# Kernel optimization log

Measured on AMD Instinct MI355X. Metric: run time of the kernel, lower is better.

## Reference

```python
import jax, jax.numpy as jnp
import numpy as np

N = 50000      # nodes
E = 800000     # edges
D = 128        # in_dim == out_dim
H = 8          # heads
DH = D // H    # head dim = 16
BN_EPS = 1e-5


def batch_norm(x, gamma, beta):
    # BatchNorm1d in training mode: biased variance over the node/batch axis.
    mu = jnp.mean(x, axis=0)
    var = jnp.mean((x - mu) ** 2, axis=0)
    return (x - mu) * jax.lax.rsqrt(var + BN_EPS) * gamma + beta


def setup_inputs() -> dict:
    key = jax.random.key(0)
    ks = jax.random.split(key, 16)
    inp = {
        'src': jax.random.randint(ks[0], (E,), 0, N),
        'dst': jax.random.randint(ks[1], (E,), 0, N),
        'h': jax.random.normal(ks[2], (N, D), jnp.float32),
        'e': jax.random.normal(ks[3], (E, D), jnp.float32),
        'h_in': jax.random.normal(ks[4], (N, D), jnp.float32),  # unused: overwritten by h in forward
        # attention projections (bias=False)
        'Wq': jax.random.normal(ks[5], (D, D), jnp.float32) / np.sqrt(D),
        'Wk': jax.random.normal(ks[6], (D, D), jnp.float32) / np.sqrt(D),
        'Wv': jax.random.normal(ks[7], (D, D), jnp.float32) / np.sqrt(D),
        'We': jax.random.normal(ks[8], (D, D), jnp.float32) / np.sqrt(D),
        # sdp_layer (bias=True)
        'W_sdp': jax.random.normal(ks[9], (D, D), jnp.float32) / np.sqrt(D),
        'b_sdp': jnp.zeros((D,), jnp.float32),
        # FFN out_h / out_h_2
        'W_h1': jax.random.normal(ks[10], (D, 2 * D), jnp.float32) / np.sqrt(D),
        'b_h1': jnp.zeros((2 * D,), jnp.float32),
        'W_h2': jax.random.normal(ks[11], (2 * D, D), jnp.float32) / np.sqrt(2 * D),
        'b_h2': jnp.zeros((D,), jnp.float32),
        # batch_norm_1 (shared across both BN applications)
        'bn_gamma': jnp.ones((D,), jnp.float32),
        'bn_beta': jnp.zeros((D,), jnp.float32),
    }
    return inp


def reference(src, dst, h, e, h_in, Wq, Wk, Wv, We, W_sdp, b_sdp,
              W_h1, b_h1, W_h2, b_h2, bn_gamma, bn_beta):
    h_res = h  # h_in = h inside forward

    # --- MultiHeadAttention (default path: all edges real, sum aggregation) ---
    q = (h @ Wq).reshape(N, H, DH)
    k = (h @ Wk).reshape(N, H, DH)
    v = (h @ Wv).reshape(N, H, DH)   # v = v_linear(h_in) with h_in == h
    ef = (e @ We).reshape(E, H, DH)

    # src_dot_dst -> scaling -> imp_exp_attn: elementwise K_src*Q_dst / sqrt(dh) * E
    score = (k[src] * q[dst]) / np.sqrt(DH) * ef          # [E, H, DH]
    # exp('score'): exp(clamp(sum_d score, -5, 5)), keepdim
    score_soft = jnp.exp(jnp.clip(score.sum(-1), -5.0, 5.0))[..., None]  # [E, H, 1]

    aV = jax.ops.segment_sum(v[src] * score_soft, dst, num_segments=N)   # [N, H, DH]
    z = jax.ops.segment_sum(score_soft, dst, num_segments=N)             # [N, H, 1]
    h_attn = (aV / (z + 1e-6)).reshape(N, D)

    # --- EncoderLayer post-attention (dropout=0 -> identity) ---
    hx = h_attn @ W_sdp + b_sdp
    hx = h_res + hx
    hx = batch_norm(hx, bn_gamma, bn_beta)

    h_in2 = hx
    ff = jax.nn.relu(hx @ W_h1 + b_h1) @ W_h2 + b_h2
    hx = h_in2 + ff
    hx = batch_norm(hx, bn_gamma, bn_beta)

    # edge_learning=False: e returned unchanged
    return hx, e
```

## Files before the change

### kernel.cpp

```cpp
#include <hip/hip_runtime.h>
#include <hip/hip_bf16.h>
#include <math.h>

#define N_NODES 50000
#define E_EDGES 800000
#define D_DIM   128
#define H_HEADS 8

typedef __attribute__((ext_vector_type(8))) short short8;
typedef __attribute__((ext_vector_type(4))) float f32x4;
typedef unsigned int   uint_t;
typedef unsigned short ushort_t;

static __device__ __forceinline__ float4 ldg4(const float* p) {
    return *reinterpret_cast<const float4*>(p);
}
static __device__ __forceinline__ ushort_t f2bf(float x) {
    union { float f; uint_t u; } v; v.f = x;
    uint_t r = v.u + 0x7fffu + ((v.u >> 16) & 1u);
    return (ushort_t)(r >> 16);
}
static __device__ __forceinline__ float bf2f(ushort_t b) {
    union { uint_t u; float f; } v; v.u = ((uint_t)b) << 16;
    return v.f;
}
static __device__ __forceinline__ uint_t pk(float lo, float hi) {
    return (uint_t)f2bf(lo) | ((uint_t)f2bf(hi) << 16);
}

__global__ void hist_kernel(const int* __restrict__ dst, int* __restrict__ hist) {
    int i = blockIdx.x * blockDim.x + threadIdx.x;
    if (i < E_EDGES) atomicAdd(&hist[dst[i]], 1);
}

__global__ __launch_bounds__(1024) void scan_kernel(const int* __restrict__ cnt,
                                                    int* __restrict__ start,
                                                    int* __restrict__ cursor) {
    __shared__ int sh[1024];
    const int t = threadIdx.x;
    const int CPT = (N_NODES + 1023) / 1024;
    int lo = t * CPT;
    int hi = lo + CPT; if (hi > N_NODES) hi = N_NODES; if (lo > N_NODES) lo = N_NODES;
    int s = 0;
    for (int i = lo; i < hi; i++) s += cnt[i];
    sh[t] = s;
    __syncthreads();
    for (int off = 1; off < 1024; off <<= 1) {
        int v = (t >= off) ? sh[t - off] : 0;
        __syncthreads();
        sh[t] += v;
        __syncthreads();
    }
    int run = sh[t] - s;
    for (int i = lo; i < hi; i++) {
        start[i]  = run;
        cursor[i] = run;
        run += cnt[i];
    }
    if (t == 1023) start[N_NODES] = sh[1023];
}

__global__ void scatter_kernel(const int* __restrict__ src, const int* __restrict__ dst,
                               int* __restrict__ cursor,
                               int* __restrict__ rank, int* __restrict__ srcs) {
    int i = blockIdx.x * blockDim.x + threadIdx.x;
    if (i < E_EDGES) {
        int p = atomicAdd(&cursor[dst[i]], 1);
        rank[i] = p;
        srcs[p] = src[i];
    }
}

__global__ __launch_bounds__(256) void prep_weights(const float* __restrict__ Wq,
                                                    const float* __restrict__ Wk,
                                                    const float* __restrict__ Wv,
                                                    const float* __restrict__ We,
                                                    const float* __restrict__ Wsdp,
                                                    const float* __restrict__ Wh1,
                                                    const float* __restrict__ Wh2,
                                                    ushort_t* __restrict__ prep) {
    const int b = blockIdx.x;
    const float* W; int ld, cb, kc;
    if (b < 6)       { W = (b < 2 ? Wq : (b < 4 ? Wk : Wv)); ld = 128; cb = 0; kc = b & 1; }
    else if (b < 8)  { W = We;   ld = 128; cb = 0;            kc = b - 6; }
    else if (b < 10) { W = Wsdp; ld = 128; cb = 0;            kc = b - 8; }
    else if (b < 14) { W = Wh1;  ld = 256; cb = (b - 10) >> 1; kc = (b - 10) & 1; }
    else             { W = Wh2;  ld = 128; cb = 0;            kc = b - 14; }
    char* tile = (char*)(prep + (size_t)b * 8192);
    for (int i = threadIdx.x; i < 8192; i += 256) {
        int col = i >> 6, kl = i & 63;
        int k = kc * 64 + kl;
        float v = W[(size_t)k * ld + cb * 128 + col];
        int byte = (col * 128 + kl * 2) ^ ((col & 7) << 4);
        *(ushort_t*)(tile + byte) = f2bf(v);
    }
}

__global__ __launch_bounds__(256) void prep_we_frag(const float* __restrict__ We,
                                                    ushort_t* __restrict__ WeF) {
    int slot = blockIdx.x * 256 + threadIdx.x;
    if (slot < 2048) {
        int lane = slot & 63;
        int kc   = (slot >> 6) & 3;
        int cg   = slot >> 8;
        int col  = cg * 16 + (lane & 15);
        int kb   = kc * 32 + ((lane >> 4) << 3);
#pragma unroll
        for (int j = 0; j < 8; j++)
            WeF[slot * 8 + j] = f2bf(We[(size_t)(kb + j) * 128 + col]);
    }
}

template<int ROWS, int OBF>
__global__ __launch_bounds__(256) void gemm_bf16(const float* __restrict__ A,
                                                 int M, int K,
                                                 const ushort_t* __restrict__ Bt, int nkc,
                                                 const float* __restrict__ bias,
                                                 const float* __restrict__ resid,
                                                 void* __restrict__ Cv, int ldc,
                                                 size_t cbStride, int doRelu) {
    constexpr int MI  = ROWS / 32;
    constexpr int TPR = 256 / ROWS;
    constexpr int KPT = 64 / TPR;
    __shared__ __align__(16) unsigned char As[ROWS * 128];
    __shared__ __align__(16) unsigned char Bs[16384];
    const int tid  = threadIdx.x;
    const int lane = tid & 63;
    const int wid  = tid >> 6;
    const int wr   = wid >> 1;
    const int wc   = wid & 1;
    const int cb   = blockIdx.y;
    const int row0 = blockIdx.x * ROWS;

    f32x4 acc[MI][4];
#pragma unroll
    for (int i = 0; i < MI; i++)
#pragma unroll
        for (int j = 0; j < 4; j++) acc[i][j] = (f32x4){0.f, 0.f, 0.f, 0.f};

    for (int kc = 0; kc < nkc; kc++) {
        __syncthreads();
        {
            int row = tid / TPR;
            int kl0 = (tid % TPR) * KPT;
            int gr  = row0 + row;
            float4 v4[KPT / 4];
            if (gr < M) {
                const float* ap = &A[(size_t)gr * K + kc * 64 + kl0];
#pragma unroll
                for (int j = 0; j < KPT / 4; j++) v4[j] = ldg4(ap + 4 * j);
            } else {
#pragma unroll
                for (int j = 0; j < KPT / 4; j++) v4[j] = make_float4(0.f, 0.f, 0.f, 0.f);
            }
            int s = (row & 7) << 4;
#pragma unroll
            for (int j = 0; j < KPT / 8; j++) {
                uint4 w;
                w.x = pk(v4[2 * j].x, v4[2 * j].y);
                w.y = pk(v4[2 * j].z, v4[2 * j].w);
                w.z = pk(v4[2 * j + 1].x, v4[2 * j + 1].y);
                w.w = pk(v4[2 * j + 1].z, v4[2 * j + 1].w);
                int byte = (row * 128 + (kl0 + 8 * j) * 2) ^ s;
                *(uint4*)(As + byte) = w;
            }
        }
        {
            const uint4* gB = (const uint4*)(Bt + (size_t)(cb * nkc + kc) * 8192);
#pragma unroll
            for (int j = 0; j < 4; j++) {
                int idx = j * 256 + tid;
                ((uint4*)Bs)[idx] = gB[idx];
            }
        }
        __syncthreads();
#pragma unroll
        for (int k0 = 0; k0 < 64; k0 += 32) {
            short8 a[MI], b[4];
#pragma unroll
            for (int mi = 0; mi < MI; mi++) {
                int row = wr * (ROWS / 2) + mi * 16 + (lane & 15);
                int byte = (row * 128 + k0 * 2 + (lane >> 4) * 16) ^ ((row & 7) << 4);
                a[mi] = *(const short8*)(As + byte);
            }
#pragma unroll
            for (int ni = 0; ni < 4; ni++) {
                int col = wc * 64 + ni * 16 + (lane & 15);
                int byte = (col * 128 + k0 * 2 + (lane >> 4) * 16) ^ ((col & 7) << 4);
                b[ni] = *(const short8*)(Bs + byte);
            }
#pragma unroll
            for (int mi = 0; mi < MI; mi++)
#pragma unroll
                for (int ni = 0; ni < 4; ni++)
                    acc[mi][ni] = __builtin_amdgcn_mfma_f32_16x16x32_bf16(a[mi], b[ni], acc[mi][ni], 0, 0, 0);
        }
    }
#pragma unroll
    for (int mi = 0; mi < MI; mi++) {
#pragma unroll
        for (int r = 0; r < 4; r++) {
            int row = row0 + wr * (ROWS / 2) + mi * 16 + ((lane >> 4) << 2) + r;
            if (row < M) {
#pragma unroll
                for (int ni = 0; ni < 4; ni++) {
                    int col = wc * 64 + ni * 16 + (lane & 15);
                    float v = acc[mi][ni][r];
                    if (bias) v += bias[cb * 128 + col];
                    if (doRelu) v = fmaxf(v, 0.f);
                    if (resid) v += resid[(size_t)row * ldc + col];
                    if (OBF) {
                        ((ushort_t*)Cv)[cb * cbStride + (size_t)row * ldc + col] = f2bf(v);
                    } else {
                        ((float*)Cv)[cb * cbStride + (size_t)row * ldc + col] = v;
                    }
                }
            }
        }
    }
}

__global__ __launch_bounds__(512, 8) void edge_mfma(const float* __restrict__ e,
                                                    const int* __restrict__ src,
                                                    const int* __restrict__ dst,
                                                    const ushort_t* __restrict__ Qm,
                                                    const ushort_t* __restrict__ Km,
                                                    const ushort_t* __restrict__ WeF,
                                                    const int* __restrict__ rank,
                                                    float* __restrict__ S,
                                                    float* __restrict__ out_e) {
    __shared__ __align__(16) unsigned char Asm[16384];
    __shared__ float sm[64][8];
    const int tid  = threadIdx.x;
    const int lane = tid & 63;
    const int wid  = tid >> 6;
    const int wr   = wid >> 2;
    const int wc   = wid & 3;
    const int e0   = blockIdx.x * 64;

    {
        int row = tid >> 3;
        int c0  = (tid & 7) * 16;
        const float* ep = &e[(size_t)(e0 + row) * 128 + c0];
        float*       op = &out_e[(size_t)(e0 + row) * 128 + c0];
        float4 v4[4];
#pragma unroll
        for (int j = 0; j < 4; j++) v4[j] = ldg4(ep + 4 * j);
#pragma unroll
        for (int j = 0; j < 4; j++) *(float4*)(op + 4 * j) = v4[j];
        int chunk = c0 >> 6;
        int klb   = (c0 & 63) * 2;
        int s     = (row & 7) << 4;
        uint4 w0, w1;
        w0.x = pk(v4[0].x, v4[0].y); w0.y = pk(v4[0].z, v4[0].w);
        w0.z = pk(v4[1].x, v4[1].y); w0.w = pk(v4[1].z, v4[1].w);
        w1.x = pk(v4[2].x, v4[2].y); w1.y = pk(v4[2].z, v4[2].w);
        w1.z = pk(v4[3].x, v4[3].y); w1.w = pk(v4[3].z, v4[3].w);
        *(uint4*)(Asm + chunk * 8192 + ((row * 128 + klb) ^ s))      = w0;
        *(uint4*)(Asm + chunk * 8192 + ((row * 128 + klb + 16) ^ s)) = w1;
    }
    __syncthreads();

    f32x4 acc[2][2];
#pragma unroll
    for (int i = 0; i < 2; i++)
#pragma unroll
        for (int j = 0; j < 2; j++) acc[i][j] = (f32x4){0.f, 0.f, 0.f, 0.f};

#pragma unroll
    for (int k0 = 0; k0 < 128; k0 += 32) {
        int chunk = k0 >> 6;
        int klb   = (k0 & 63) * 2;
        int kc    = k0 >> 5;
        short8 a[2];
#pragma unroll
        for (int mi = 0; mi < 2; mi++) {
            int arow = wr * 32 + mi * 16 + (lane & 15);
            int byte = chunk * 8192 + ((arow * 128 + klb + (lane >> 4) * 16) ^ ((arow & 7) << 4));
            a[mi] = *(const short8*)(Asm + byte);
        }
#pragma unroll
        for (int ni = 0; ni < 2; ni++) {
            int cg = wc * 2 + ni;
            short8 b = *(const short8*)(WeF + ((size_t)((cg * 4 + kc) * 64 + lane)) * 8);
#pragma unroll
            for (int mi = 0; mi < 2; mi++)
                acc[mi][ni] = __builtin_amdgcn_mfma_f32_16x16x32_bf16(a[mi], b, acc[mi][ni], 0, 0, 0);
        }
    }

#pragma unroll
    for (int mi = 0; mi < 2; mi++) {
        int rows[4], sidx[4], didx[4];
#pragma unroll
        for (int r = 0; r < 4; r++) {
            rows[r] = e0 + wr * 32 + mi * 16 + ((lane >> 4) << 2) + r;
            sidx[r] = src[rows[r]];
            didx[r] = dst[rows[r]];
        }
#pragma unroll
        for (int ni = 0; ni < 2; ni++) {
            int head = wc * 2 + ni;
            int col  = head * 16 + (lane & 15);
            float pv[4];
#pragma unroll
            for (int r = 0; r < 4; r++) {
                float kv = bf2f(Km[(size_t)sidx[r] * 128 + col]);
                float qv = bf2f(Qm[(size_t)didx[r] * 128 + col]);
                pv[r] = acc[mi][ni][r] * kv * qv;
            }
#pragma unroll
            for (int off = 1; off < 16; off <<= 1)
#pragma unroll
                for (int r = 0; r < 4; r++) pv[r] += __shfl_xor(pv[r], off, 64);
            if ((lane & 15) == 0) {
#pragma unroll
                for (int r = 0; r < 4; r++) {
                    float v = fminf(fmaxf(0.25f * pv[r], -5.f), 5.f);
                    sm[rows[r] - e0][head] = __expf(v);
                }
            }
        }
    }
    __syncthreads();
    if (tid < 64) {
        int rk = rank[e0 + tid];
        float4 a0 = *(const float4*)&sm[tid][0];
        float4 a1 = *(const float4*)&sm[tid][4];
        *(float4*)&S[(size_t)rk * 8]     = a0;
        *(float4*)&S[(size_t)rk * 8 + 4] = a1;
    }
}

__global__ __launch_bounds__(128) void agg_kernel(const ushort_t* __restrict__ V,
                                                  const float* __restrict__ S,
                                                  const int* __restrict__ start,
                                                  const int* __restrict__ srcs,
                                                  float* __restrict__ HA) {
    const int n = blockIdx.x;
    const int t = threadIdx.x;
    const int h = t >> 4;
    const int s0 = start[n];
    const int s1 = start[n + 1];
    float acc = 0.f, z = 0.f;
    int i = s0;
    for (; i + 4 <= s1; i += 4) {
        int  n0 = srcs[i], n1 = srcs[i + 1], n2 = srcs[i + 2], n3 = srcs[i + 3];
        float sv0 = S[(size_t)i * 8 + h];
        float sv1 = S[(size_t)(i + 1) * 8 + h];
        float sv2 = S[(size_t)(i + 2) * 8 + h];
        float sv3 = S[(size_t)(i + 3) * 8 + h];
        float v0 = bf2f(V[(size_t)n0 * 128 + t]);
        float v1 = bf2f(V[(size_t)n1 * 128 + t]);
        float v2 = bf2f(V[(size_t)n2 * 128 + t]);
        float v3 = bf2f(V[(size_t)n3 * 128 + t]);
        acc = fmaf(sv0, v0, acc); acc = fmaf(sv1, v1, acc);
        acc = fmaf(sv2, v2, acc); acc = fmaf(sv3, v3, acc);
        z += sv0 + sv1 + sv2 + sv3;
    }
    for (; i < s1; i++) {
        int ns = srcs[i];
        float sv = S[(size_t)i * 8 + h];
        acc = fmaf(sv, bf2f(V[(size_t)ns * 128 + t]), acc);
        z += sv;
    }
    HA[(size_t)n * 128 + t] = acc / (z + 1e-6f);
}

__global__ __launch_bounds__(256) void bn_stats(const float* __restrict__ X,
                                                float* __restrict__ sums) {
    __shared__ float s1[256], s2[256];
    const int tid = threadIdx.x;
    float a1 = 0.f, a2 = 0.f;
    const size_t total = (size_t)N_NODES * 128;
    for (size_t i = (size_t)blockIdx.x * 256 + tid; i < total; i += (size_t)gridDim.x * 256) {
        float v = X[i];
        a1 += v;
        a2 += v * v;
    }
    s1[tid] = a1; s2[tid] = a2;
    __syncthreads();
    if (tid < 128) {
        a1 = s1[tid] + s1[tid + 128];
        a2 = s2[tid] + s2[tid + 128];
        atomicAdd(&sums[tid], a1);
        atomicAdd(&sums[128 + tid], a2);
    }
}

__global__ void bn_finalize(const float* __restrict__ sums, float* __restrict__ mu_rstd) {
    int c = threadIdx.x;
    float mu  = sums[c] * (1.f / (float)N_NODES);
    float var = sums[128 + c] * (1.f / (float)N_NODES) - mu * mu;
    mu_rstd[c]       = mu;
    mu_rstd[128 + c] = rsqrtf(var + 1e-5f);
}

__global__ __launch_bounds__(256) void bn_apply(const float* __restrict__ X,
                                                const float* __restrict__ mu_rstd,
                                                const float* __restrict__ gamma,
                                                const float* __restrict__ beta,
                                                float* __restrict__ Y) {
    const size_t total = (size_t)N_NODES * 128;
    const size_t step = (size_t)gridDim.x * blockDim.x * 4;
    for (size_t i = ((size_t)blockIdx.x * blockDim.x + threadIdx.x) * 4; i < total; i += step) {
        float4 x = ldg4(&X[i]);
        int c = (int)(i & 127);
        float4 y;
        y.x = (x.x - mu_rstd[c + 0]) * mu_rstd[128 + c + 0] * gamma[c + 0] + beta[c + 0];
        y.y = (x.y - mu_rstd[c + 1]) * mu_rstd[128 + c + 1] * gamma[c + 1] + beta[c + 1];
        y.z = (x.z - mu_rstd[c + 2]) * mu_rstd[128 + c + 2] * gamma[c + 2] + beta[c + 2];
        y.w = (x.w - mu_rstd[c + 3]) * mu_rstd[128 + c + 3] * gamma[c + 3] + beta[c + 3];
        *reinterpret_cast<float4*>(&Y[i]) = y;
    }
}

extern "C" void kernel_launch(void* const* d_in, const int* in_sizes, int n_in,
                              void* d_out, int out_size, void* d_ws, size_t ws_size,
                              hipStream_t stream) {
    (void)in_sizes; (void)n_in; (void)out_size; (void)ws_size;
    const int*   src   = (const int*)d_in[0];
    const int*   dst   = (const int*)d_in[1];
    const float* h     = (const float*)d_in[2];
    const float* e     = (const float*)d_in[3];
    const float* Wq    = (const float*)d_in[5];
    const float* Wk    = (const float*)d_in[6];
    const float* Wv    = (const float*)d_in[7];
    const float* We    = (const float*)d_in[8];
    const float* Wsdp  = (const float*)d_in[9];
    const float* bsdp  = (const float*)d_in[10];
    const float* Wh1   = (const float*)d_in[11];
    const float* bh1   = (const float*)d_in[12];
    const float* Wh2   = (const float*)d_in[13];
    const float* bh2   = (const float*)d_in[14];
    const float* gamma = (const float*)d_in[15];
    const float* beta  = (const float*)d_in[16];
    float* out = (float*)d_out;

    float* ws = (float*)d_ws;
    const size_t NM = (size_t)N_NODES * 128;
    float* Qb    = ws;
    float* Kb    = ws + NM;
    float* Vb    = ws + 2 * NM;
    float* Sb    = ws + 3 * NM;
    float* T1    = ws + 4 * NM;
    float* STATS = ws + 6 * NM;
    int* hist   = (int*)(STATS + 1024);
    int* startp = hist + N_NODES;
    int* cursor = startp + N_NODES + 1;
    ushort_t* prep = (ushort_t*)(((uintptr_t)(cursor + N_NODES) + 255) & ~(uintptr_t)255);
    ushort_t* WeF  = prep + (size_t)18 * 8192;

    ushort_t* Q16 = (ushort_t*)Qb;
    ushort_t* K16 = Q16 + NM;
    ushort_t* V16 = Q16 + 2 * NM;

    int* rank = (int*)T1;
    int* srcs = rank + E_EDGES;

    float* sums1 = STATS;
    float* mr1   = STATS + 256;
    float* sums2 = STATS + 512;
    float* mr2   = STATS + 768;

    prep_weights<<<18, 256, 0, stream>>>(Wq, Wk, Wv, We, Wsdp, Wh1, Wh2, prep);
    prep_we_frag<<<8, 256, 0, stream>>>(We, WeF);

    hipMemsetAsync(STATS, 0, (1024 + N_NODES) * sizeof(float), stream);

    hist_kernel<<<(E_EDGES + 255) / 256, 256, 0, stream>>>(dst, hist);
    scan_kernel<<<1, 1024, 0, stream>>>(hist, startp, cursor);
    scatter_kernel<<<(E_EDGES + 255) / 256, 256, 0, stream>>>(src, dst, cursor, rank, srcs);

    const int rt128 = (N_NODES + 127) / 128;
    const int rt64  = (N_NODES + 63) / 64;

    gemm_bf16<128, 1><<<dim3(rt128, 3), 256, 0, stream>>>(h, N_NODES, 128, prep, 2,
                                                          nullptr, nullptr, Q16, 128, NM, 0);

    edge_mfma<<<E_EDGES / 64, 512, 0, stream>>>(e, src, dst, Q16, K16, WeF,
                                                rank, Sb, out + NM);

    agg_kernel<<<N_NODES, 128, 0, stream>>>(V16, Sb, startp, srcs, Vb);

    gemm_bf16<64, 0><<<dim3(rt64, 1), 256, 0, stream>>>(Vb, N_NODES, 128, prep + (size_t)8 * 8192, 2,
                                                        bsdp, h, Kb, 128, 0, 0);

    bn_stats<<<512, 256, 0, stream>>>(Kb, sums1);
    bn_finalize<<<1, 128, 0, stream>>>(sums1, mr1);
    bn_apply<<<2048, 256, 0, stream>>>(Kb, mr1, gamma, beta, Qb);

    gemm_bf16<128, 0><<<dim3(rt128, 2), 256, 0, stream>>>(Qb, N_NODES, 128, prep + (size_t)10 * 8192, 2,
                                                          bh1, nullptr, T1, 256, 128, 1);
    gemm_bf16<64, 0><<<dim3(rt64, 1), 256, 0, stream>>>(T1, N_NODES, 256, prep + (size_t)14 * 8192, 4,
                                                        bh2, Qb, Kb, 128, 0, 0);

    bn_stats<<<512, 256, 0, stream>>>(Kb, sums2);
    bn_finalize<<<1, 128, 0, stream>>>(sums2, mr2);
    bn_apply<<<2048, 256, 0, stream>>>(Kb, mr2, gamma, beta, out);
}
```

Baseline: 800.2 us.

## Make edge kernel persistent over four tiles with double-buffered LDS prefetch

Each edge block now walks four 64-edge tiles instead of one. It keeps two LDS staging buffers and issues the global load of the next tile's edge features and rank while the current tile's MFMA and gather work runs. The goal is to hide global-load latency and cut per-block launch and sync overhead. In exchange, LDS use doubles, there are four times fewer blocks, and the launch-bounds occupancy hint drops from 8 to 6.

After: 1.007 ms. +25.9%, slower.

```diff
diff --git a/kernel.cpp b/kernel.cpp
--- a/kernel.cpp
+++ b/kernel.cpp
@@ -6,6 +6,7 @@
 #define E_EDGES 800000
 #define D_DIM   128
 #define H_HEADS 8
+#define ETILES  4
 
 typedef __attribute__((ext_vector_type(8))) short short8;
 typedef __attribute__((ext_vector_type(4))) float f32x4;
@@ -220,7 +221,21 @@
     }
 }
 
-__global__ __launch_bounds__(512, 8) void edge_mfma(const float* __restrict__ e,
+static __device__ __forceinline__ void stage_tile(unsigned char* buf, int row, int c0,
+                                                  const float4* v4) {
+    int chunk = c0 >> 6;
+    int klb   = (c0 & 63) * 2;
+    int s     = (row & 7) << 4;
+    uint4 w0, w1;
+    w0.x = pk(v4[0].x, v4[0].y); w0.y = pk(v4[0].z, v4[0].w);
+    w0.z = pk(v4[1].x, v4[1].y); w0.w = pk(v4[1].z, v4[1].w);
+    w1.x = pk(v4[2].x, v4[2].y); w1.y = pk(v4[2].z, v4[2].w);
+    w1.z = pk(v4[3].x, v4[3].y); w1.w = pk(v4[3].z, v4[3].w);
+    *(uint4*)(buf + chunk * 8192 + ((row * 128 + klb) ^ s))      = w0;
+    *(uint4*)(buf + chunk * 8192 + ((row * 128 + klb + 16) ^ s)) = w1;
+}
+
+__global__ __launch_bounds__(512, 6) void edge_mfma(const float* __restrict__ e,
                                                     const int* __restrict__ src,
                                                     const int* __restrict__ dst,
                                                     const ushort_t* __restrict__ Qm,
@@ -229,106 +244,119 @@
                                                     const int* __restrict__ rank,
                                                     float* __restrict__ S,
                                                     float* __restrict__ out_e) {
-    __shared__ __align__(16) unsigned char Asm[16384];
+    __shared__ __align__(16) unsigned char Asm[2][16384];
     __shared__ float sm[64][8];
     const int tid  = threadIdx.x;
     const int lane = tid & 63;
     const int wid  = tid >> 6;
     const int wr   = wid >> 2;
     const int wc   = wid & 3;
-    const int e0   = blockIdx.x * 64;
-
+    const int row  = tid >> 3;
+    const int c0   = (tid & 7) * 16;
+    const int base = blockIdx.x * (64 * ETILES);
+
+    int rk = (tid < 64) ? rank[base + tid] : 0;
     {
-        int row = tid >> 3;
-        int c0  = (tid & 7) * 16;
-        const float* ep = &e[(size_t)(e0 + row) * 128 + c0];
-        float*       op = &out_e[(size_t)(e0 + row) * 128 + c0];
+        const float* ep = &e[(size_t)(base + row) * 128 + c0];
         float4 v4[4];
 #pragma unroll
         for (int j = 0; j < 4; j++) v4[j] = ldg4(ep + 4 * j);
+        float* op = &out_e[(size_t)(base + row) * 128 + c0];
 #pragma unroll
         for (int j = 0; j < 4; j++) *(float4*)(op + 4 * j) = v4[j];
-        int chunk = c0 >> 6;
-        int klb   = (c0 & 63) * 2;
-        int s     = (row & 7) << 4;
-        uint4 w0, w1;
-        w0.x = pk(v4[0].x, v4[0].y); w0.y = pk(v4[0].z, v4[0].w);
-        w0.z = pk(v4[1].x, v4[1].y); w0.w = pk(v4[1].z, v4[1].w);
-        w1.x = pk(v4[2].x, v4[2].y); w1.y = pk(v4[2].z, v4[2].w);
-        w1.z = pk(v4[3].x, v4[3].y); w1.w = pk(v4[3].z, v4[3].w);
-        *(uint4*)(Asm + chunk * 8192 + ((row * 128 + klb) ^ s))      = w0;
-        *(uint4*)(Asm + chunk * 8192 + ((row * 128 + klb + 16) ^ s)) = w1;
-    }
-    __syncthreads();
-
-    f32x4 acc[2][2];
-#pragma unroll
-    for (int i = 0; i < 2; i++)
-#pragma unroll
-        for (int j = 0; j < 2; j++) acc[i][j] = (f32x4){0.f, 0.f, 0.f, 0.f};
-
-#pragma unroll
-    for (int k0 = 0; k0 < 128; k0 += 32) {
-        int chunk = k0 >> 6;
-        int klb   = (k0 & 63) * 2;
-        int kc    = k0 >> 5;
-        short8 a[2];
+        stage_tile(Asm[0], row, c0, v4);
+    }
+
+#pragma unroll 1
+    for (int t = 0; t < ETILES; t++) {
+        const int e0 = base + t * 64;
+        __syncthreads();
+
+        float4 nv[4];
+        if (t + 1 < ETILES) {
+            const float* ep = &e[(size_t)(e0 + 64 + row) * 128 + c0];
+#pragma unroll
+            for (int j = 0; j < 4; j++) nv[j] = ldg4(ep + 4 * j);
+        }
+        int rk_cur = rk;
+        if (t + 1 < ETILES && tid < 64) rk = rank[e0 + 64 + tid];
+
+        f32x4 acc[2][2];
+#pragma unroll
+        for (int i = 0; i < 2; i++)
+#pragma unroll
+            for (int j = 0; j < 2; j++) acc[i][j] = (f32x4){0.f, 0.f, 0.f, 0.f};
+        const unsigned char* buf = Asm[t & 1];
+#pragma unroll
+        for (int k0 = 0; k0 < 128; k0 += 32) {
+            int chunk = k0 >> 6;
+            int klb   = (k0 & 63) * 2;
+            int kc    = k0 >> 5;
+            short8 a[2];
+#pragma unroll
+            for (int mi = 0; mi < 2; mi++) {
+                int arow = wr * 32 + mi * 16 + (lane & 15);
+                int byte = chunk * 8192 + ((arow * 128 + klb + (lane >> 4) * 16) ^ ((arow & 7) << 4));
+                a[mi] = *(const short8*)(buf + byte);
+            }
+#pragma unroll
+            for (int ni = 0; ni < 2; ni++) {
+                int cg = wc * 2 + ni;
+                short8 b = *(const short8*)(WeF + ((size_t)((cg * 4 + kc) * 64 + lane)) * 8);
+#pragma unroll
+                for (int mi = 0; mi < 2; mi++)
+                    acc[mi][ni] = __builtin_amdgcn_mfma_f32_16x16x32_bf16(a[mi], b, acc[mi][ni], 0, 0, 0);
+            }
+        }
+
 #pragma unroll
         for (int mi = 0; mi < 2; mi++) {
-            int arow = wr * 32 + mi * 16 + (lane & 15);
-            int byte = chunk * 8192 + ((arow * 128 + klb + (lane >> 4) * 16) ^ ((arow & 7) << 4));
-            a[mi] = *(const short8*)(Asm + byte);
-        }
-#pragma unroll
-        for (int ni = 0; ni < 2; ni++) {
-            int cg = wc * 2 + ni;
-            short8 b = *(const short8*)(WeF + ((size_t)((cg * 4 + kc) * 64 + lane)) * 8);
-#pragma unroll
-            for (int mi = 0; mi < 2; mi++)
-                acc[mi][ni] = __builtin_amdgcn_mfma_f32_16x16x32_bf16(a[mi], b, acc[mi][ni], 0, 0, 0);
-        }
-    }
-
-#pragma unroll
-    for (int mi = 0; mi < 2; mi++) {
-        int rows[4], sidx[4], didx[4];
-#pragma unroll
-        for (int r = 0; r < 4; r++) {
-            rows[r] = e0 + wr * 32 + mi * 16 + ((lane >> 4) << 2) + r;
-            sidx[r] = src[rows[r]];
-            didx[r] = dst[rows[r]];
-        }
-#pragma unroll
-        for (int ni = 0; ni < 2; ni++) {
-            int head = wc * 2 + ni;
-            int col  = head * 16 + (lane & 15);
-            float pv[4];
+            int rows[4], sidx[4], didx[4];
 #pragma unroll
             for (int r = 0; r < 4; r++) {
-                float kv = bf2f(Km[(size_t)sidx[r] * 128 + col]);
-                float qv = bf2f(Qm[(size_t)didx[r] * 128 + col]);
-                pv[r] = acc[mi][ni][r] * kv * qv;
-            }
-#pragma unroll
-            for (int off = 1; off < 16; off <<= 1)
-#pragma unroll
-                for (int r = 0; r < 4; r++) pv[r] += __shfl_xor(pv[r], off, 64);
-            if ((lane & 15) == 0) {
+                rows[r] = e0 + wr * 32 + mi * 16 + ((lane >> 4) << 2) + r;
+                sidx[r] = src[rows[r]];
+                didx[r] = dst[rows[r]];
+            }
+#pragma unroll
+            for (int ni = 0; ni < 2; ni++) {
+                int head = wc * 2 + ni;
+                int col  = head * 16 + (lane & 15);
+                float pv[4];
 #pragma unroll
                 for (int r = 0; r < 4; r++) {
-                    float v = fminf(fmaxf(0.25f * pv[r], -5.f), 5.f);
-                    sm[rows[r] - e0][head] = __expf(v);
+                    float kv = bf2f(Km[(size_t)sidx[r] * 128 + col]);
+                    float qv = bf2f(Qm[(size_t)didx[r] * 128 + col]);
+                    pv[r] = acc[mi][ni][r] * kv * qv;
                 }
-            }
-        }
-    }
-    __syncthreads();
-    if (tid < 64) {
-        int rk = rank[e0 + tid];
-        float4 a0 = *(const float4*)&sm[tid][0];
-        float4 a1 = *(const float4*)&sm[tid][4];
-        *(float4*)&S[(size_t)rk * 8]     = a0;
-        *(float4*)&S[(size_t)rk * 8 + 4] = a1;
+#pragma unroll
+                for (int off = 1; off < 16; off <<= 1)
+#pragma unroll
+                    for (int r = 0; r < 4; r++) pv[r] += __shfl_xor(pv[r], off, 64);
+                if ((lane & 15) == 0) {
+#pragma unroll
+                    for (int r = 0; r < 4; r++) {
+                        float v = fminf(fmaxf(0.25f * pv[r], -5.f), 5.f);
+                        sm[rows[r] - e0][head] = __expf(v);
+                    }
+                }
+            }
+        }
+        __syncthreads();
+
+        if (tid < 64) {
+            float4 a0 = *(const float4*)&sm[tid][0];
+            float4 a1 = *(const float4*)&sm[tid][4];
+            *(float4*)&S[(size_t)rk_cur * 8]     = a0;
+            *(float4*)&S[(size_t)rk_cur * 8 + 4] = a1;
+        }
+
+        if (t + 1 < ETILES) {
+            float* op = &out_e[(size_t)(e0 + 64 + row) * 128 + c0];
+#pragma unroll
+            for (int j = 0; j < 4; j++) *(float4*)(op + 4 * j) = nv[j];
+            stage_tile(Asm[(t + 1) & 1], row, c0, nv);
+        }
     }
 }
 
@@ -478,8 +506,8 @@
     gemm_bf16<128, 1><<<dim3(rt128, 3), 256, 0, stream>>>(h, N_NODES, 128, prep, 2,
                                                           nullptr, nullptr, Q16, 128, NM, 0);
 
-    edge_mfma<<<E_EDGES / 64, 512, 0, stream>>>(e, src, dst, Q16, K16, WeF,
-                                                rank, Sb, out + NM);
+    edge_mfma<<<E_EDGES / (64 * ETILES), 512, 0, stream>>>(e, src, dst, Q16, K16, WeF,
+                                                           rank, Sb, out + NM);
 
     agg_kernel<<<N_NODES, 128, 0, stream>>>(V16, Sb, startp, srcs, Vb);
 
```

## Fuse BN statistics into GEMM epilogues and store intermediates in bf16

Applied to the files above, without the earlier changes.

The BatchNorm column sums and sums of squares are now accumulated in the epilogues of the sdp and FFN2 GEMMs, so the two standalone bn_stats passes are gone. The aggregation output, the normalized activations and the FFN hidden layer are stored as bf16, and the GEMM loads bf16 A and residual inputs directly, which roughly halves intermediate memory traffic. The aggregation kernel now maps one wave per node with packed bf16 pairs, and bn_finalize folds gamma and beta into a single scale and shift. In exchange, the bf16 intermediates and residual lose precision, and per-block shared and global float atomics change the order of summation.

New measurement: 754.6 us. -5.7%, faster.

```diff
diff --git a/kernel.cpp b/kernel.cpp
--- a/kernel.cpp
+++ b/kernel.cpp
@@ -111,19 +111,21 @@
     }
 }
 
-template<int ROWS, int OBF>
-__global__ __launch_bounds__(256) void gemm_bf16(const float* __restrict__ A,
+template<int ROWS, int OBF, int ABF, int RBF, int SADD>
+__global__ __launch_bounds__(256) void gemm_bf16(const void* __restrict__ Av,
                                                  int M, int K,
                                                  const ushort_t* __restrict__ Bt, int nkc,
                                                  const float* __restrict__ bias,
-                                                 const float* __restrict__ resid,
+                                                 const void* __restrict__ residv,
                                                  void* __restrict__ Cv, int ldc,
-                                                 size_t cbStride, int doRelu) {
+                                                 size_t cbStride, int doRelu,
+                                                 float* __restrict__ sums) {
     constexpr int MI  = ROWS / 32;
     constexpr int TPR = 256 / ROWS;
     constexpr int KPT = 64 / TPR;
     __shared__ __align__(16) unsigned char As[ROWS * 128];
     __shared__ __align__(16) unsigned char Bs[16384];
+    __shared__ float csum[128], csq[128];
     const int tid  = threadIdx.x;
     const int lane = tid & 63;
     const int wid  = tid >> 6;
@@ -132,6 +134,8 @@
     const int cb   = blockIdx.y;
     const int row0 = blockIdx.x * ROWS;
 
+    if (SADD && tid < 128) { csum[tid] = 0.f; csq[tid] = 0.f; }
+
     f32x4 acc[MI][4];
 #pragma unroll
     for (int i = 0; i < MI; i++)
@@ -144,25 +148,37 @@
             int row = tid / TPR;
             int kl0 = (tid % TPR) * KPT;
             int gr  = row0 + row;
-            float4 v4[KPT / 4];
-            if (gr < M) {
-                const float* ap = &A[(size_t)gr * K + kc * 64 + kl0];
-#pragma unroll
-                for (int j = 0; j < KPT / 4; j++) v4[j] = ldg4(ap + 4 * j);
+            int s = (row & 7) << 4;
+            if (ABF) {
+                const ushort_t* A16 = (const ushort_t*)Av;
+#pragma unroll
+                for (int j = 0; j < KPT / 8; j++) {
+                    uint4 w = make_uint4(0, 0, 0, 0);
+                    if (gr < M) w = *(const uint4*)(&A16[(size_t)gr * K + kc * 64 + kl0 + 8 * j]);
+                    int byte = (row * 128 + (kl0 + 8 * j) * 2) ^ s;
+                    *(uint4*)(As + byte) = w;
+                }
             } else {
-#pragma unroll
-                for (int j = 0; j < KPT / 4; j++) v4[j] = make_float4(0.f, 0.f, 0.f, 0.f);
-            }
-            int s = (row & 7) << 4;
-#pragma unroll
-            for (int j = 0; j < KPT / 8; j++) {
-                uint4 w;
-                w.x = pk(v4[2 * j].x, v4[2 * j].y);
-                w.y = pk(v4[2 * j].z, v4[2 * j].w);
-                w.z = pk(v4[2 * j + 1].x, v4[2 * j + 1].y);
-                w.w = pk(v4[2 * j + 1].z, v4[2 * j + 1].w);
-                int byte = (row * 128 + (kl0 + 8 * j) * 2) ^ s;
-                *(uint4*)(As + byte) = w;
+                const float* A = (const float*)Av;
+                float4 v4[KPT / 4];
+                if (gr < M) {
+                    const float* ap = &A[(size_t)gr * K + kc * 64 + kl0];
+#pragma unroll
+                    for (int j = 0; j < KPT / 4; j++) v4[j] = ldg4(ap + 4 * j);
+                } else {
+#pragma unroll
+                    for (int j = 0; j < KPT / 4; j++) v4[j] = make_float4(0.f, 0.f, 0.f, 0.f);
+                }
+#pragma unroll
+                for (int j = 0; j < KPT / 8; j++) {
+                    uint4 w;
+                    w.x = pk(v4[2 * j].x, v4[2 * j].y);
+                    w.y = pk(v4[2 * j].z, v4[2 * j].w);
+                    w.z = pk(v4[2 * j + 1].x, v4[2 * j + 1].y);
+                    w.w = pk(v4[2 * j + 1].z, v4[2 * j + 1].w);
+                    int byte = (row * 128 + (kl0 + 8 * j) * 2) ^ s;
+                    *(uint4*)(As + byte) = w;
+                }
             }
         }
         {
@@ -196,6 +212,9 @@
                     acc[mi][ni] = __builtin_amdgcn_mfma_f32_16x16x32_bf16(a[mi], b[ni], acc[mi][ni], 0, 0, 0);
         }
     }
+
+    float colS[4] = {0.f, 0.f, 0.f, 0.f};
+    float colQ[4] = {0.f, 0.f, 0.f, 0.f};
 #pragma unroll
     for (int mi = 0; mi < MI; mi++) {
 #pragma unroll
@@ -208,14 +227,28 @@
                     float v = acc[mi][ni][r];
                     if (bias) v += bias[cb * 128 + col];
                     if (doRelu) v = fmaxf(v, 0.f);
-                    if (resid) v += resid[(size_t)row * ldc + col];
-                    if (OBF) {
-                        ((ushort_t*)Cv)[cb * cbStride + (size_t)row * ldc + col] = f2bf(v);
-                    } else {
-                        ((float*)Cv)[cb * cbStride + (size_t)row * ldc + col] = v;
+                    if (residv) {
+                        if (RBF) v += bf2f(((const ushort_t*)residv)[(size_t)row * ldc + col]);
+                        else     v += ((const float*)residv)[(size_t)row * ldc + col];
                     }
+                    if (SADD) { colS[ni] += v; colQ[ni] += v * v; }
+                    if (OBF) ((ushort_t*)Cv)[cb * cbStride + (size_t)row * ldc + col] = f2bf(v);
+                    else     ((float*)Cv)[cb * cbStride + (size_t)row * ldc + col] = v;
                 }
             }
+        }
+    }
+    if (SADD) {
+#pragma unroll
+        for (int ni = 0; ni < 4; ni++) {
+            int col = wc * 64 + ni * 16 + (lane & 15);
+            atomicAdd(&csum[col], colS[ni]);
+            atomicAdd(&csq[col],  colQ[ni]);
+        }
+        __syncthreads();
+        if (tid < 128) {
+            atomicAdd(&sums[tid],       csum[tid]);
+            atomicAdd(&sums[128 + tid], csq[tid]);
         }
     }
 }
@@ -332,86 +365,81 @@
     }
 }
 
-__global__ __launch_bounds__(128) void agg_kernel(const ushort_t* __restrict__ V,
+__global__ __launch_bounds__(256) void agg_kernel(const uint_t* __restrict__ Vu,
                                                   const float* __restrict__ S,
                                                   const int* __restrict__ start,
                                                   const int* __restrict__ srcs,
-                                                  float* __restrict__ HA) {
-    const int n = blockIdx.x;
-    const int t = threadIdx.x;
-    const int h = t >> 4;
+                                                  uint_t* __restrict__ HAu) {
+    const int lane = threadIdx.x & 63;
+    const int n = blockIdx.x * 4 + (threadIdx.x >> 6);
+    if (n >= N_NODES) return;
     const int s0 = start[n];
     const int s1 = start[n + 1];
-    float acc = 0.f, z = 0.f;
+    const int h  = lane >> 3;
+    float a0 = 0.f, a1 = 0.f, z = 0.f;
     int i = s0;
     for (; i + 4 <= s1; i += 4) {
-        int  n0 = srcs[i], n1 = srcs[i + 1], n2 = srcs[i + 2], n3 = srcs[i + 3];
-        float sv0 = S[(size_t)i * 8 + h];
-        float sv1 = S[(size_t)(i + 1) * 8 + h];
-        float sv2 = S[(size_t)(i + 2) * 8 + h];
-        float sv3 = S[(size_t)(i + 3) * 8 + h];
-        float v0 = bf2f(V[(size_t)n0 * 128 + t]);
-        float v1 = bf2f(V[(size_t)n1 * 128 + t]);
-        float v2 = bf2f(V[(size_t)n2 * 128 + t]);
-        float v3 = bf2f(V[(size_t)n3 * 128 + t]);
-        acc = fmaf(sv0, v0, acc); acc = fmaf(sv1, v1, acc);
-        acc = fmaf(sv2, v2, acc); acc = fmaf(sv3, v3, acc);
-        z += sv0 + sv1 + sv2 + sv3;
+        int m0 = srcs[i], m1 = srcs[i + 1], m2 = srcs[i + 2], m3 = srcs[i + 3];
+        float t0 = S[(size_t)i * 8 + h];
+        float t1 = S[(size_t)(i + 1) * 8 + h];
+        float t2 = S[(size_t)(i + 2) * 8 + h];
+        float t3 = S[(size_t)(i + 3) * 8 + h];
+        uint_t v0 = Vu[(size_t)m0 * 64 + lane];
+        uint_t v1 = Vu[(size_t)m1 * 64 + lane];
+        uint_t v2 = Vu[(size_t)m2 * 64 + lane];
+        uint_t v3 = Vu[(size_t)m3 * 64 + lane];
+        a0 = fmaf(t0, bf2f((ushort_t)v0), a0); a1 = fmaf(t0, bf2f((ushort_t)(v0 >> 16)), a1);
+        a0 = fmaf(t1, bf2f((ushort_t)v1), a0); a1 = fmaf(t1, bf2f((ushort_t)(v1 >> 16)), a1);
+        a0 = fmaf(t2, bf2f((ushort_t)v2), a0); a1 = fmaf(t2, bf2f((ushort_t)(v2 >> 16)), a1);
+        a0 = fmaf(t3, bf2f((ushort_t)v3), a0); a1 = fmaf(t3, bf2f((ushort_t)(v3 >> 16)), a1);
+        z += t0 + t1 + t2 + t3;
     }
     for (; i < s1; i++) {
-        int ns = srcs[i];
-        float sv = S[(size_t)i * 8 + h];
-        acc = fmaf(sv, bf2f(V[(size_t)ns * 128 + t]), acc);
-        z += sv;
-    }
-    HA[(size_t)n * 128 + t] = acc / (z + 1e-6f);
-}
-
-__global__ __launch_bounds__(256) void bn_stats(const float* __restrict__ X,
-                                                float* __restrict__ sums) {
-    __shared__ float s1[256], s2[256];
-    const int tid = threadIdx.x;
-    float a1 = 0.f, a2 = 0.f;
-    const size_t total = (size_t)N_NODES * 128;
-    for (size_t i = (size_t)blockIdx.x * 256 + tid; i < total; i += (size_t)gridDim.x * 256) {
-        float v = X[i];
-        a1 += v;
-        a2 += v * v;
-    }
-    s1[tid] = a1; s2[tid] = a2;
-    __syncthreads();
-    if (tid < 128) {
-        a1 = s1[tid] + s1[tid + 128];
-        a2 = s2[tid] + s2[tid + 128];
-        atomicAdd(&sums[tid], a1);
-        atomicAdd(&sums[128 + tid], a2);
-    }
-}
-
-__global__ void bn_finalize(const float* __restrict__ sums, float* __restrict__ mu_rstd) {
+        int m = srcs[i];
+        float t = S[(size_t)i * 8 + h];
+        uint_t v = Vu[(size_t)m * 64 + lane];
+        a0 = fmaf(t, bf2f((ushort_t)v), a0);
+        a1 = fmaf(t, bf2f((ushort_t)(v >> 16)), a1);
+        z += t;
+    }
+    float inv = 1.f / (z + 1e-6f);
+    HAu[(size_t)n * 64 + lane] = pk(a0 * inv, a1 * inv);
+}
+
+__global__ void bn_finalize(const float* __restrict__ sums,
+                            const float* __restrict__ gamma,
+                            const float* __restrict__ beta,
+                            float* __restrict__ ss) {
     int c = threadIdx.x;
     float mu  = sums[c] * (1.f / (float)N_NODES);
     float var = sums[128 + c] * (1.f / (float)N_NODES) - mu * mu;
-    mu_rstd[c]       = mu;
-    mu_rstd[128 + c] = rsqrtf(var + 1e-5f);
-}
-
+    float scale = rsqrtf(var + 1e-5f) * gamma[c];
+    ss[c]       = scale;
+    ss[128 + c] = beta[c] - mu * scale;
+}
+
+template<int OBF>
 __global__ __launch_bounds__(256) void bn_apply(const float* __restrict__ X,
-                                                const float* __restrict__ mu_rstd,
-                                                const float* __restrict__ gamma,
-                                                const float* __restrict__ beta,
-                                                float* __restrict__ Y) {
+                                                const float* __restrict__ ss,
+                                                void* __restrict__ Yv) {
     const size_t total = (size_t)N_NODES * 128;
     const size_t step = (size_t)gridDim.x * blockDim.x * 4;
     for (size_t i = ((size_t)blockIdx.x * blockDim.x + threadIdx.x) * 4; i < total; i += step) {
         float4 x = ldg4(&X[i]);
         int c = (int)(i & 127);
         float4 y;
-        y.x = (x.x - mu_rstd[c + 0]) * mu_rstd[128 + c + 0] * gamma[c + 0] + beta[c + 0];
-        y.y = (x.y - mu_rstd[c + 1]) * mu_rstd[128 + c + 1] * gamma[c + 1] + beta[c + 1];
-        y.z = (x.z - mu_rstd[c + 2]) * mu_rstd[128 + c + 2] * gamma[c + 2] + beta[c + 2];
-        y.w = (x.w - mu_rstd[c + 3]) * mu_rstd[128 + c + 3] * gamma[c + 3] + beta[c + 3];
-        *reinterpret_cast<float4*>(&Y[i]) = y;
+        y.x = x.x * ss[c + 0] + ss[128 + c + 0];
+        y.y = x.y * ss[c + 1] + ss[128 + c + 1];
+        y.z = x.z * ss[c + 2] + ss[128 + c + 2];
+        y.w = x.w * ss[c + 3] + ss[128 + c + 3];
+        if (OBF) {
+            uint2 p;
+            p.x = pk(y.x, y.y);
+            p.y = pk(y.z, y.w);
+            *(uint2*)((ushort_t*)Yv + i) = p;
+        } else {
+            *(float4*)((float*)Yv + i) = y;
+        }
     }
 }
 
@@ -439,29 +467,29 @@
 
     float* ws = (float*)d_ws;
     const size_t NM = (size_t)N_NODES * 128;
-    float* Qb    = ws;
-    float* Kb    = ws + NM;
-    float* Vb    = ws + 2 * NM;
-    float* Sb    = ws + 3 * NM;
-    float* T1    = ws + 4 * NM;
-    float* STATS = ws + 6 * NM;
+    ushort_t* Q16  = (ushort_t*)ws;
+    ushort_t* K16  = Q16 + NM;
+    ushort_t* V16  = Q16 + 2 * NM;
+    ushort_t* HA16 = (ushort_t*)(ws + 3 * NM / 2);
+    float*    Kb   = ws + 2 * NM;
+    float*    Sb   = ws + 3 * NM;
+    float*    T1r  = ws + 4 * NM;
+    ushort_t* T16  = (ushort_t*)T1r;
+    ushort_t* Qb16 = (ushort_t*)(ws + 5 * NM);
+    float*    STATS = ws + 6 * NM;
     int* hist   = (int*)(STATS + 1024);
     int* startp = hist + N_NODES;
     int* cursor = startp + N_NODES + 1;
     ushort_t* prep = (ushort_t*)(((uintptr_t)(cursor + N_NODES) + 255) & ~(uintptr_t)255);
     ushort_t* WeF  = prep + (size_t)18 * 8192;
 
-    ushort_t* Q16 = (ushort_t*)Qb;
-    ushort_t* K16 = Q16 + NM;
-    ushort_t* V16 = Q16 + 2 * NM;
-
-    int* rank = (int*)T1;
+    int* rank = (int*)T1r;
     int* srcs = rank + E_EDGES;
 
     float* sums1 = STATS;
-    float* mr1   = STATS + 256;
+    float* ss1   = STATS + 256;
     float* sums2 = STATS + 512;
-    float* mr2   = STATS + 768;
+    float* ss2   = STATS + 768;
 
     prep_weights<<<18, 256, 0, stream>>>(Wq, Wk, Wv, We, Wsdp, Wh1, Wh2, prep);
     prep_we_frag<<<8, 256, 0, stream>>>(We, WeF);
@@ -475,27 +503,26 @@
     const int rt128 = (N_NODES + 127) / 128;
     const int rt64  = (N_NODES + 63) / 64;
 
-    gemm_bf16<128, 1><<<dim3(rt128, 3), 256, 0, stream>>>(h, N_NODES, 128, prep, 2,
-                                                          nullptr, nullptr, Q16, 128, NM, 0);
+    gemm_bf16<128, 1, 0, 0, 0><<<dim3(rt128, 3), 256, 0, stream>>>(
+        h, N_NODES, 128, prep, 2, nullptr, nullptr, Q16, 128, NM, 0, nullptr);
 
     edge_mfma<<<E_EDGES / 64, 512, 0, stream>>>(e, src, dst, Q16, K16, WeF,
                                                 rank, Sb, out + NM);
 
-    agg_kernel<<<N_NODES, 128, 0, stream>>>(V16, Sb, startp, srcs, Vb);
-
-    gemm_bf16<64, 0><<<dim3(rt64, 1), 256, 0, stream>>>(Vb, N_NODES, 128, prep + (size_t)8 * 8192, 2,
-                                                        bsdp, h, Kb, 128, 0, 0);
-
-    bn_stats<<<512, 256, 0, stream>>>(Kb, sums1);
-    bn_finalize<<<1, 128, 0, stream>>>(sums1, mr1);
-    bn_apply<<<2048, 256, 0, stream>>>(Kb, mr1, gamma, beta, Qb);
-
-    gemm_bf16<128, 0><<<dim3(rt128, 2), 256, 0, stream>>>(Qb, N_NODES, 128, prep + (size_t)10 * 8192, 2,
-                                                          bh1, nullptr, T1, 256, 128, 1);
-    gemm_bf16<64, 0><<<dim3(rt64, 1), 256, 0, stream>>>(T1, N_NODES, 256, prep + (size_t)14 * 8192, 4,
-                                                        bh2, Qb, Kb, 128, 0, 0);
-
-    bn_stats<<<512, 256, 0, stream>>>(Kb, sums2);
-    bn_finalize<<<1, 128, 0, stream>>>(sums2, mr2);
-    bn_apply<<<2048, 256, 0, stream>>>(Kb, mr2, gamma, beta, out);
-}
+    agg_kernel<<<(N_NODES + 3) / 4, 256, 0, stream>>>((const uint_t*)V16, Sb, startp, srcs,
+                                                      (uint_t*)HA16);
+
+    gemm_bf16<64, 0, 1, 0, 1><<<dim3(rt64, 1), 256, 0, stream>>>(
+        HA16, N_NODES, 128, prep + (size_t)8 * 8192, 2, bsdp, h, Kb, 128, 0, 0, sums1);
+
+    bn_finalize<<<1, 128, 0, stream>>>(sums1, gamma, beta, ss1);
+    bn_apply<1><<<2048, 256, 0, stream>>>(Kb, ss1, Qb16);
+
+    gemm_bf16<128, 1, 1, 0, 0><<<dim3(rt128, 2), 256, 0, stream>>>(
+        Qb16, N_NODES, 128, prep + (size_t)10 * 8192, 2, bh1, nullptr, T16, 256, 128, 1, nullptr);
+    gemm_bf16<64, 0, 1, 1, 1><<<dim3(rt64, 1), 256, 0, stream>>>(
+        T16, N_NODES, 256, prep + (size_t)14 * 8192, 4, bh2, Qb16, Kb, 128, 0, 0, sums2);
+
+    bn_finalize<<<1, 128, 0, stream>>>(sums2, gamma, beta, ss2);
+    bn_apply<0><<<2048, 256, 0, stream>>>(Kb, ss2, out);
+}
```
